# Optimization experiments

Hardware: AMD Instinct MI355X
Metric: run time of the kernel (lower is better)

## Reference

```python
import jax, jax.numpy as jnp
import numpy as np

STRIDE = 3


def _conv_block(x, W, b):
    # x: (B, L, C) -> windows (B, L-2, 3C) via fixed-stride slicing (faithful to scan_conv)
    B, L, C = x.shape
    Lw = L - STRIDE + 1
    win = jnp.concatenate([x[:, i:Lw + i, :] for i in range(STRIDE)], axis=-1)  # (B, Lw, 3C)
    y = jax.nn.leaky_relu(jnp.einsum('blk,ok->blo', win, W) + b)  # torch Linear: x @ W.T + b
    # zero_gate: zero rows of the *window* tensor zero the output
    mask = (jnp.sum(win, axis=2, keepdims=True) != 0).astype(y.dtype)
    y = y * mask
    # max_pool1d over sequence, kernel=2 stride=2 (floor)
    Lp = y.shape[1] // 2
    y = y[:, :2 * Lp, :].reshape(B, Lp, 2, -1).max(axis=2)
    return y


def setup_inputs() -> dict:
    key = jax.random.key(0)
    ks = jax.random.split(key, 16)
    B, PAD, E, IMG, V = 1024, 30, 512, 2048, 32000
    c1, c2, c3, lin2 = 200, 300, 300, 400
    lin1_in = 2 * c3 + IMG  # flattened (B,2,300) + image -> 600 + 2048
    s = 0.02
    return {
        'image_vectors': jax.random.normal(ks[0], (B, IMG), jnp.float32),
        'sentences': jax.random.randint(ks[1], (B, PAD), 0, V, jnp.int32),
        'embed_table': jax.random.normal(ks[2], (V, E), jnp.float32),
        'W1': jax.random.normal(ks[3], (c1, E * STRIDE), jnp.float32) * s,
        'b1': jnp.zeros((c1,), jnp.float32),
        'W2': jax.random.normal(ks[4], (c2, c1 * STRIDE), jnp.float32) * s,
        'b2': jnp.zeros((c2,), jnp.float32),
        'W3': jax.random.normal(ks[5], (c3, c2 * STRIDE), jnp.float32) * s,
        'b3': jnp.zeros((c3,), jnp.float32),
        'Wm': jax.random.normal(ks[6], (lin2, lin1_in), jnp.float32) * s,
        'bm': jnp.zeros((lin2,), jnp.float32),
        'Wo': jax.random.normal(ks[7], (1, lin2), jnp.float32) * s,
        'bo': jnp.zeros((1,), jnp.float32),
    }


def reference(image_vectors, sentences, embed_table, W1, b1, W2, b2, W3, b3, Wm, bm, Wo, bo):
    x = embed_table[sentences]                       # (B, 30, 512)
    x = _conv_block(x, W1, b1)                       # (B, 14, 200)
    x = _conv_block(x, W2, b2)                       # (B, 6, 300)
    x = _conv_block(x, W3, b3)                       # (B, 2, 300)
    B = x.shape[0]
    feats = jnp.concatenate([x.reshape(B, -1), image_vectors], axis=1)  # (B, 2648)
    h = jax.nn.leaky_relu(feats @ Wm.T + bm)         # (B, 400)
    out = h @ Wo.T + bo                              # (B, 1)
    return out
```

## Files before the change

### kernel.cpp

```cpp
#include <hip/hip_runtime.h>
#include <hip/hip_bf16.h>

#define LEAKY(v) ((v) > 0.0f ? (v) : 0.01f * (v))

constexpr int B_   = 1024;
constexpr int PAD  = 30;
constexpr int E    = 512;
constexpr int IMG  = 2048;
constexpr int C1   = 200;
constexpr int C2   = 300;
constexpr int C3   = 300;
constexpr int LIN2 = 400;

constexpr int NT1P = 16, KT1 = 48;
constexpr int NT2P = 20, KT2 = 21;
constexpr int NT3P = 24, KT3 = 30;
constexpr int NTMP = 28, KTM = 83;
constexpr int FK  = 2656;

constexpr int T1 = NT1P * KT1;
constexpr int T2 = NT2P * KT2;
constexpr int T3 = NT3P * KT3;
constexpr int TM = NTMP * KTM;
constexpr int TTOT = T1 + T2 + T3 + TM;

typedef __attribute__((ext_vector_type(8))) short bf16x8;
typedef __attribute__((ext_vector_type(4))) float f32x4;

__device__ inline unsigned short f2bf(float f) {
    __hip_bfloat16 h = __float2bfloat16(f);
    return *reinterpret_cast<unsigned short*>(&h);
}
__device__ inline float bf2f(unsigned short u) {
    unsigned int b = ((unsigned int)u) << 16;
    return __uint_as_float(b);
}

__global__ __launch_bounds__(256) void convert_all(
    const float* __restrict__ W1, const float* __restrict__ W2,
    const float* __restrict__ W3, const float* __restrict__ Wm,
    unsigned short* __restrict__ W1t, unsigned short* __restrict__ W2t,
    unsigned short* __restrict__ W3t, unsigned short* __restrict__ Wmt)
{
    int idx = blockIdx.x * 256 + threadIdx.x;
    if (idx >= TTOT * 64) return;
    int lane = idx & 63, t = idx >> 6;
    unsigned short v[8];

    if (t < T1) {
        int kk = t % KT1, nt = t / KT1;
        int ch = nt * 16 + (lane & 15);
        int k0 = kk * 32 + (lane >> 4) * 8;
        #pragma unroll
        for (int j = 0; j < 8; ++j)
            v[j] = (ch < C1) ? f2bf(W1[(size_t)ch * (3*E) + k0 + j]) : (unsigned short)0;
        ushort4* dst = reinterpret_cast<ushort4*>(W1t) + (size_t)t * 128 + lane * 2;
        dst[0] = ushort4{v[0],v[1],v[2],v[3]};
        dst[1] = ushort4{v[4],v[5],v[6],v[7]};
    } else if (t < T1 + T2) {
        int tt = t - T1;
        int kk = tt % KT2, nt = tt / KT2;
        int ch = nt * 16 + (lane & 15);
        int rowoff = kk / 7;
        int cbase  = (kk % 7) * 32 + (lane >> 4) * 8;
        #pragma unroll
        for (int j = 0; j < 8; ++j) {
            int c = cbase + j;
            v[j] = (ch < C2 && c < C1) ? f2bf(W2[(size_t)ch * (3*C1) + rowoff * C1 + c])
                                       : (unsigned short)0;
        }
        ushort4* dst = reinterpret_cast<ushort4*>(W2t) + (size_t)tt * 128 + lane * 2;
        dst[0] = ushort4{v[0],v[1],v[2],v[3]};
        dst[1] = ushort4{v[4],v[5],v[6],v[7]};
    } else if (t < T1 + T2 + T3) {
        int tt = t - T1 - T2;
        int kk = tt % KT3, nt = tt / KT3;
        int ch = nt * 16 + (lane & 15);
        int rowoff = kk / 10;
        int cbase  = (kk % 10) * 32 + (lane >> 4) * 8;
        #pragma unroll
        for (int j = 0; j < 8; ++j) {
            int c = cbase + j;
            v[j] = (ch < C3 && c < C2) ? f2bf(W3[(size_t)ch * (3*C2) + rowoff * C2 + c])
                                       : (unsigned short)0;
        }
        ushort4* dst = reinterpret_cast<ushort4*>(W3t) + (size_t)tt * 128 + lane * 2;
        dst[0] = ushort4{v[0],v[1],v[2],v[3]};
        dst[1] = ushort4{v[4],v[5],v[6],v[7]};
    } else {
        int tt = t - T1 - T2 - T3;
        int kk = tt % KTM, nt = tt / KTM;
        int ch = nt * 16 + (lane & 15);
        int kbase = kk * 32 + (lane >> 4) * 8;
        #pragma unroll
        for (int j = 0; j < 8; ++j) {
            int k = kbase + j;
            v[j] = (ch < LIN2 && k < 2648) ? f2bf(Wm[(size_t)ch * 2648 + k])
                                           : (unsigned short)0;
        }
        ushort4* dst = reinterpret_cast<ushort4*>(Wmt) + (size_t)tt * 128 + lane * 2;
        dst[0] = ushort4{v[0],v[1],v[2],v[3]};
        dst[1] = ushort4{v[4],v[5],v[6],v[7]};
    }
}

__global__ __launch_bounds__(512, 4) void conv1_mfma(
    const int* __restrict__ sent, const float* __restrict__ emb,
    const unsigned short* __restrict__ W1t, const float* __restrict__ bias,
    float* __restrict__ y)
{
    const int blk = blockIdx.x;
    const int tid = threadIdx.x;
    __shared__ unsigned short xs[66 * 512];
    __shared__ float rs[64];
    char* xsb = reinterpret_cast<char*>(xs);

    const int wid = tid >> 6, lane = tid & 63;

    for (int r = wid; r < 60; r += 8) {
        int bl = r / 30, rr = r % 30;
        int R = bl * 32 + rr;
        int row = sent[(2 * blk + bl) * PAD + rr];
        const float4* src = reinterpret_cast<const float4*>(emb + (size_t)row * E) + lane * 2;
        float4 e0 = src[0], e1 = src[1];
        float sum = e0.x + e0.y + e0.z + e0.w + e1.x + e1.y + e1.z + e1.w;
        union { ushort4 u4[2]; bf16x8 v; } pk;
        pk.u4[0] = ushort4{f2bf(e0.x), f2bf(e0.y), f2bf(e0.z), f2bf(e0.w)};
        pk.u4[1] = ushort4{f2bf(e1.x), f2bf(e1.y), f2bf(e1.z), f2bf(e1.w)};
        int byteoff = R * 1024 + ((lane ^ (R & 7)) << 4);
        *reinterpret_cast<bf16x8*>(xsb + byteoff) = pk.v;
        for (int off = 32; off; off >>= 1) sum += __shfl_down(sum, off);
        if (lane == 0) rs[R] = sum;
    }
    if (tid < 384) {
        int zi = tid >> 6;
        int R = (zi < 2) ? (30 + zi) : (60 + zi);
        int byteoff = R * 1024 + ((lane ^ (R & 7)) << 4);
        union { ushort4 u4[2]; bf16x8 v; } pk;
        pk.u4[0] = ushort4{0,0,0,0}; pk.u4[1] = ushort4{0,0,0,0};
        *reinterpret_cast<bf16x8*>(xsb + byteoff) = pk.v;
    }
    if (tid < 4) {
        const int pr[4] = {30, 31, 62, 63};
        rs[pr[tid]] = 0.f;
    }
    __syncthreads();

    const int kg = lane >> 4, trow = lane & 15, g = kg;

    const bf16x8* wb = reinterpret_cast<const bf16x8*>(W1t);
    const bf16x8* wp0 = wb + (size_t)((wid    ) * KT1) * 64 + lane;
    const bf16x8* wp1 = wb + (size_t)((wid + 8) * KT1) * 64 + lane;

    f32x4 c00={0,0,0,0},c01={0,0,0,0},c02={0,0,0,0},c03={0,0,0,0};
    f32x4 c10={0,0,0,0},c11={0,0,0,0},c12={0,0,0,0},c13={0,0,0,0};

    #pragma unroll
    for (int rowoff = 0; rowoff < 3; ++rowoff) {
        const int R0 = trow + rowoff;
        const int R1 = R0 + 16, R2 = R0 + 32, R3 = R0 + 48;
        const int b3_0 = R0 * 1024 + (((R0 & 7) ^ kg) << 4);
        const int b3_1 = R1 * 1024 + (((R1 & 7) ^ kg) << 4);
        const int b3_2 = R2 * 1024 + (((R2 & 7) ^ kg) << 4);
        const int b3_3 = R3 * 1024 + (((R3 & 7) ^ kg) << 4);
        #pragma unroll
        for (int cc = 0; cc < 16; ++cc) {
            const int kk = rowoff * 16 + cc;
            bf16x8 a0 = *reinterpret_cast<const bf16x8*>(xsb + (b3_0 ^ (cc << 6)));
            bf16x8 a1 = *reinterpret_cast<const bf16x8*>(xsb + (b3_1 ^ (cc << 6)));
            bf16x8 a2 = *reinterpret_cast<const bf16x8*>(xsb + (b3_2 ^ (cc << 6)));
            bf16x8 a3 = *reinterpret_cast<const bf16x8*>(xsb + (b3_3 ^ (cc << 6)));
            bf16x8 b0 = wp0[kk * 64];
            bf16x8 b1 = wp1[kk * 64];
            c00 = __builtin_amdgcn_mfma_f32_16x16x32_bf16(a0, b0, c00, 0, 0, 0);
            c01 = __builtin_amdgcn_mfma_f32_16x16x32_bf16(a1, b0, c01, 0, 0, 0);
            c02 = __builtin_amdgcn_mfma_f32_16x16x32_bf16(a2, b0, c02, 0, 0, 0);
            c03 = __builtin_amdgcn_mfma_f32_16x16x32_bf16(a3, b0, c03, 0, 0, 0);
            c10 = __builtin_amdgcn_mfma_f32_16x16x32_bf16(a0, b1, c10, 0, 0, 0);
            c11 = __builtin_amdgcn_mfma_f32_16x16x32_bf16(a1, b1, c11, 0, 0, 0);
            c12 = __builtin_amdgcn_mfma_f32_16x16x32_bf16(a2, b1, c12, 0, 0, 0);
            c13 = __builtin_amdgcn_mfma_f32_16x16x32_bf16(a3, b1, c13, 0, 0, 0);
        }
    }

#define EPIM1(MT, CM) do {                                                       \
    int bl = (MT) >> 1;                                                          \
    int mloc = ((MT) & 1) * 16;                                                  \
    int bb = 2 * blk + bl;                                                       \
    _Pragma("unroll")                                                            \
    for (int hf = 0; hf < 2; ++hf) {                                             \
        int wl = mloc + 4 * g + 2 * hf;                                          \
        int tp = wl >> 1;                                                        \
        if (tp < 14) {                                                           \
            float v0 = CM[2*hf] + bia, v1 = CM[2*hf+1] + bia;                    \
            v0 = LEAKY(v0); v1 = LEAKY(v1);                                      \
            int rb = bl * 32 + wl;                                               \
            if (rs[rb] + rs[rb+1] + rs[rb+2] == 0.f) v0 = 0.f;                   \
            if (rs[rb+1] + rs[rb+2] + rs[rb+3] == 0.f) v1 = 0.f;                 \
            y[(size_t)(bb * 14 + tp) * C1 + ch] = fmaxf(v0, v1);                 \
        }                                                                        \
    }                                                                            \
} while (0)

#define EPI1(NTI, CA, CB, CC, CD) do {                                           \
    int ch = (wid + 8 * (NTI)) * 16 + trow;                                      \
    if (ch < C1) {                                                               \
        float bia = bias[ch];                                                    \
        EPIM1(0, CA); EPIM1(1, CB); EPIM1(2, CC); EPIM1(3, CD);                  \
    }                                                                            \
} while (0)

    EPI1(0, c00, c01, c02, c03);
    EPI1(1, c10, c11, c12, c13);
#undef EPI1
#undef EPIM1
}

__global__ __launch_bounds__(256, 4) void conv2_mfma(
    const float* __restrict__ x, const unsigned short* __restrict__ Wt,
    const float* __restrict__ bias, float* __restrict__ y)
{
    const int b   = blockIdx.x;
    const int tid = threadIdx.x;
    __shared__ unsigned short xs[18 * 256];
    __shared__ float rs[18];
    char* xsb = reinterpret_cast<char*>(xs);

    for (int idx = tid; idx < 18 * 32; idx += 256) {
        int r = idx >> 5, ck = idx & 31;
        ushort4 lo = {0,0,0,0}, hi = {0,0,0,0};
        if (r < 14 && ck < 25) {
            const float4* src = reinterpret_cast<const float4*>(
                x + ((size_t)b * 14 + r) * C1 + ck * 8);
            float4 a = src[0], c = src[1];
            lo = ushort4{f2bf(a.x),f2bf(a.y),f2bf(a.z),f2bf(a.w)};
            hi = ushort4{f2bf(c.x),f2bf(c.y),f2bf(c.z),f2bf(c.w)};
        }
        int bo_ = r * 512 + ((ck ^ (r & 7)) << 4);
        *reinterpret_cast<ushort4*>(xsb + bo_)     = lo;
        *reinterpret_cast<ushort4*>(xsb + bo_ + 8) = hi;
    }
    __syncthreads();

    const int wid = tid >> 6, lane = tid & 63;
    const int kg = lane >> 4, trow = lane & 15, g = kg;

    for (int r = wid; r < 18; r += 4) {
        float s = 0.f;
        #pragma unroll
        for (int j = 0; j < 4; ++j) {
            int e = lane + 64 * j;
            int chunk = e >> 3, within = e & 7;
            s += bf2f(*reinterpret_cast<unsigned short*>(
                xsb + r * 512 + ((chunk ^ (r & 7)) << 4) + within * 2));
        }
        for (int off = 32; off; off >>= 1) s += __shfl_down(s, off);
        if (lane == 0) rs[r] = s;
    }
    __syncthreads();

    const bf16x8* wb = reinterpret_cast<const bf16x8*>(Wt);
    const bf16x8* wp0 = wb + (size_t)((wid     ) * KT2) * 64 + lane;
    const bf16x8* wp1 = wb + (size_t)((wid +  4) * KT2) * 64 + lane;
    const bf16x8* wp2 = wb + (size_t)((wid +  8) * KT2) * 64 + lane;
    const bf16x8* wp3 = wb + (size_t)((wid + 12) * KT2) * 64 + lane;
    const bf16x8* wp4 = wb + (size_t)((wid + 16) * KT2) * 64 + lane;

    f32x4 d0={0,0,0,0},d1={0,0,0,0},d2={0,0,0,0},d3={0,0,0,0},d4={0,0,0,0};

    int kidx = 0;
    #pragma unroll
    for (int rowoff = 0; rowoff < 3; ++rowoff) {
        const int R0 = trow + rowoff;
        const int b3 = R0 * 512 + (((R0 & 7) ^ kg) << 4);
        #pragma unroll
        for (int cc = 0; cc < 7; ++cc, ++kidx) {
            bf16x8 a0 = *reinterpret_cast<const bf16x8*>(xsb + (b3 ^ (cc << 6)));
            bf16x8 b0 = wp0[kidx * 64];
            bf16x8 b1 = wp1[kidx * 64];
            bf16x8 b2 = wp2[kidx * 64];
            bf16x8 b3v = wp3[kidx * 64];
            bf16x8 b4 = wp4[kidx * 64];
            d0 = __builtin_amdgcn_mfma_f32_16x16x32_bf16(a0, b0,  d0, 0, 0, 0);
            d1 = __builtin_amdgcn_mfma_f32_16x16x32_bf16(a0, b1,  d1, 0, 0, 0);
            d2 = __builtin_amdgcn_mfma_f32_16x16x32_bf16(a0, b2,  d2, 0, 0, 0);
            d3 = __builtin_amdgcn_mfma_f32_16x16x32_bf16(a0, b3v, d3, 0, 0, 0);
            d4 = __builtin_amdgcn_mfma_f32_16x16x32_bf16(a0, b4,  d4, 0, 0, 0);
        }
    }

#define EPI2(NTI, DM) do {                                                       \
    int ch = (wid + 4 * (NTI)) * 16 + trow;                                      \
    if (ch < C2) {                                                               \
        float bia = bias[ch];                                                    \
        _Pragma("unroll")                                                        \
        for (int hf = 0; hf < 2; ++hf) {                                         \
            int t0 = 4 * g + 2 * hf;                                             \
            if (t0 < 12) {                                                       \
                float v0 = LEAKY(DM[2*hf]   + bia);                              \
                float v1 = LEAKY(DM[2*hf+1] + bia);                              \
                if (rs[t0] + rs[t0+1] + rs[t0+2] == 0.f) v0 = 0.f;               \
                if (rs[t0+1] + rs[t0+2] + rs[t0+3] == 0.f) v1 = 0.f;             \
                y[((size_t)b * 6 + (t0 >> 1)) * C2 + ch] = fmaxf(v0, v1);        \
            }                                                                    \
        }                                                                        \
    }                                                                            \
} while (0)

    EPI2(0, d0);
    EPI2(1, d1);
    EPI2(2, d2);
    EPI2(3, d3);
    EPI2(4, d4);
#undef EPI2
}

__global__ __launch_bounds__(512, 4) void conv3_mfma(
    const float* __restrict__ x, const unsigned short* __restrict__ Wt,
    const float* __restrict__ bias, float* __restrict__ y)
{
    const int b0  = blockIdx.x * 4;
    const int tid = threadIdx.x;
    __shared__ unsigned short xs[24 * 320];
    __shared__ float rs[24];
    char* xsb = reinterpret_cast<char*>(xs);

    for (int idx = tid; idx < 24 * 40; idx += 512) {
        int rg = idx / 40, ck = idx % 40;
        int c0 = ck * 8;
        ushort4 lo = {0,0,0,0}, hi = {0,0,0,0};
        const float* row = x + ((size_t)b0 * 6 + rg) * C2;
        if (c0 + 8 <= C2) {
            const float4* src = reinterpret_cast<const float4*>(row + c0);
            float4 a = src[0], c = src[1];
            lo = ushort4{f2bf(a.x),f2bf(a.y),f2bf(a.z),f2bf(a.w)};
            hi = ushort4{f2bf(c.x),f2bf(c.y),f2bf(c.z),f2bf(c.w)};
        } else if (c0 < C2) {
            unsigned short v[8];
            #pragma unroll
            for (int j = 0; j < 8; ++j)
                v[j] = (c0 + j < C2) ? f2bf(row[c0 + j]) : (unsigned short)0;
            lo = ushort4{v[0],v[1],v[2],v[3]};
            hi = ushort4{v[4],v[5],v[6],v[7]};
        }
        int bo_ = rg * 640 + ((ck ^ (rg & 7)) << 4);
        *reinterpret_cast<ushort4*>(xsb + bo_)     = lo;
        *reinterpret_cast<ushort4*>(xsb + bo_ + 8) = hi;
    }
    __syncthreads();

    const int wid = tid >> 6, lane = tid & 63;
    const int kg = lane >> 4, trow = lane & 15, g = kg;

    for (int r = wid; r < 24; r += 8) {
        float s = 0.f;
        #pragma unroll
        for (int j = 0; j < 5; ++j) {
            int e = lane + 64 * j;
            int chunk = e >> 3, within = e & 7;
            s += bf2f(*reinterpret_cast<unsigned short*>(
                xsb + r * 640 + ((chunk ^ (r & 7)) << 4) + within * 2));
        }
        for (int off = 32; off; off >>= 1) s += __shfl_down(s, off);
        if (lane == 0) rs[r] = s;
    }
    __syncthreads();

    const int rbase = 6 * (trow >> 2) + (trow & 3);

    const bf16x8* wb = reinterpret_cast<const bf16x8*>(Wt);
    const bf16x8* wp0 = wb + (size_t)((wid     ) * KT3) * 64 + lane;
    const bf16x8* wp1 = wb + (size_t)((wid +  8) * KT3) * 64 + lane;
    const bf16x8* wp2 = wb + (size_t)((wid + 16) * KT3) * 64 + lane;

    f32x4 e0={0,0,0,0},e1={0,0,0,0},e2={0,0,0,0};

    int kidx = 0;
    #pragma unroll
    for (int rowoff = 0; rowoff < 3; ++rowoff) {
        const int R0 = rbase + rowoff;
        #pragma unroll
        for (int cc = 0; cc < 10; ++cc, ++kidx) {
            int chunk = cc * 4 + kg;
            bf16x8 a0 = *reinterpret_cast<const bf16x8*>(
                xsb + R0 * 640 + ((chunk ^ (R0 & 7)) << 4));
            bf16x8 b0 = wp0[kidx * 64];
            bf16x8 b1 = wp1[kidx * 64];
            bf16x8 b2 = wp2[kidx * 64];
            e0 = __builtin_amdgcn_mfma_f32_16x16x32_bf16(a0, b0, e0, 0, 0, 0);
            e1 = __builtin_amdgcn_mfma_f32_16x16x32_bf16(a0, b1, e1, 0, 0, 0);
            e2 = __builtin_amdgcn_mfma_f32_16x16x32_bf16(a0, b2, e2, 0, 0, 0);
        }
    }

#define EPI3(NTI, EM) do {                                                       \
    int ch = (wid + 8 * (NTI)) * 16 + trow;                                      \
    if (ch < C3) {                                                               \
        float bia = bias[ch];                                                    \
        _Pragma("unroll")                                                        \
        for (int tp = 0; tp < 2; ++tp) {                                         \
            int rb = g * 6 + 2 * tp;                                             \
            float v0 = LEAKY(EM[2*tp]   + bia);                                  \
            float v1 = LEAKY(EM[2*tp+1] + bia);                                  \
            if (rs[rb] + rs[rb+1] + rs[rb+2] == 0.f) v0 = 0.f;                   \
            if (rs[rb+1] + rs[rb+2] + rs[rb+3] == 0.f) v1 = 0.f;                 \
            y[((size_t)(b0 + g) * 2 + tp) * C3 + ch] = fmaxf(v0, v1);            \
        }                                                                        \
    }                                                                            \
} while (0)

    EPI3(0, e0);
    EPI3(1, e1);
    EPI3(2, e2);
#undef EPI3
}

__global__ __launch_bounds__(256) void concat_feats(
    const float* __restrict__ y3, const float* __restrict__ img,
    unsigned short* __restrict__ feats)
{
    const int b = blockIdx.x;
    for (int ck = threadIdx.x; ck < FK / 8; ck += 256) {
        int c0 = ck * 8;
        ushort4 lo = {0,0,0,0}, hi = {0,0,0,0};
        const float4* src = nullptr;
        if (c0 + 8 <= 600)       src = reinterpret_cast<const float4*>(y3 + (size_t)b*600 + c0);
        else if (c0 + 8 <= 2648) src = reinterpret_cast<const float4*>(img + (size_t)b*IMG + (c0-600));
        if (src) {
            float4 a = src[0], c = src[1];
            lo = ushort4{f2bf(a.x),f2bf(a.y),f2bf(a.z),f2bf(a.w)};
            hi = ushort4{f2bf(c.x),f2bf(c.y),f2bf(c.z),f2bf(c.w)};
        }
        ushort4* dst = reinterpret_cast<ushort4*>(feats + (size_t)b * FK + c0);
        dst[0] = lo; dst[1] = hi;
    }
}

__global__ __launch_bounds__(64) void final_mfma(
    const unsigned short* __restrict__ feats, const unsigned short* __restrict__ Wmt,
    const float* __restrict__ bm, float* __restrict__ h)
{
    const int lane = threadIdx.x;
    const int bid  = blockIdx.x;
    const int mt = bid / 7, q = bid % 7;
    const int kg = lane >> 4, trow = lane & 15, g = kg;
    const int m0 = mt * 16;

    const bf16x8* ap = reinterpret_cast<const bf16x8*>(feats)
                       + (size_t)(m0 + trow) * (FK / 8) + kg;
    const bf16x8* wb = reinterpret_cast<const bf16x8*>(Wmt);
    const bf16x8* wp0 = wb + (size_t)((q     ) * KTM) * 64 + lane;
    const bf16x8* wp1 = wb + (size_t)((q +  7) * KTM) * 64 + lane;
    const bf16x8* wp2 = wb + (size_t)((q + 14) * KTM) * 64 + lane;
    const bf16x8* wp3 = wb + (size_t)((q + 21) * KTM) * 64 + lane;

    f32x4 c0 = {0,0,0,0}, c1 = {0,0,0,0}, c2 = {0,0,0,0}, c3 = {0,0,0,0};

    bf16x8 aA = ap[0],      aB = ap[4];
    bf16x8 b0A = wp0[0],  b1A = wp1[0],  b2A = wp2[0],  b3A = wp3[0];
    bf16x8 b0B = wp0[64], b1B = wp1[64], b2B = wp2[64], b3B = wp3[64];
    for (int kk = 0; kk < KTM - 2; ++kk) {
        bf16x8 a = aA, b0 = b0A, b1 = b1A, b2 = b2A, b3 = b3A;
        aA = aB;  b0A = b0B; b1A = b1B; b2A = b2B; b3A = b3B;
        aB  = ap [(kk + 2) * 4];
        b0B = wp0[(kk + 2) * 64];
        b1B = wp1[(kk + 2) * 64];
        b2B = wp2[(kk + 2) * 64];
        b3B = wp3[(kk + 2) * 64];
        c0 = __builtin_amdgcn_mfma_f32_16x16x32_bf16(a, b0, c0, 0, 0, 0);
        c1 = __builtin_amdgcn_mfma_f32_16x16x32_bf16(a, b1, c1, 0, 0, 0);
        c2 = __builtin_amdgcn_mfma_f32_16x16x32_bf16(a, b2, c2, 0, 0, 0);
        c3 = __builtin_amdgcn_mfma_f32_16x16x32_bf16(a, b3, c3, 0, 0, 0);
    }
    c0 = __builtin_amdgcn_mfma_f32_16x16x32_bf16(aA, b0A, c0, 0, 0, 0);
    c1 = __builtin_amdgcn_mfma_f32_16x16x32_bf16(aA, b1A, c1, 0, 0, 0);
    c2 = __builtin_amdgcn_mfma_f32_16x16x32_bf16(aA, b2A, c2, 0, 0, 0);
    c3 = __builtin_amdgcn_mfma_f32_16x16x32_bf16(aA, b3A, c3, 0, 0, 0);
    c0 = __builtin_amdgcn_mfma_f32_16x16x32_bf16(aB, b0B, c0, 0, 0, 0);
    c1 = __builtin_amdgcn_mfma_f32_16x16x32_bf16(aB, b1B, c1, 0, 0, 0);
    c2 = __builtin_amdgcn_mfma_f32_16x16x32_bf16(aB, b2B, c2, 0, 0, 0);
    c3 = __builtin_amdgcn_mfma_f32_16x16x32_bf16(aB, b3B, c3, 0, 0, 0);

#define EPIM(NT, CM) do {                                                        \
    int ch = (NT) * 16 + trow;                                                   \
    if (ch < LIN2) {                                                             \
        float bia = bm[ch];                                                      \
        _Pragma("unroll")                                                        \
        for (int reg = 0; reg < 4; ++reg) {                                      \
            float v = LEAKY(CM[reg] + bia);                                      \
            h[(size_t)(m0 + 4 * g + reg) * LIN2 + ch] = v;                       \
        }                                                                        \
    }                                                                            \
} while (0)

    EPIM(q,      c0);
    EPIM(q + 7,  c1);
    EPIM(q + 14, c2);
    EPIM(q + 21, c3);
#undef EPIM
}

__global__ __launch_bounds__(256) void final_reduce(
    const float* __restrict__ h, const float* __restrict__ Wo,
    const float* __restrict__ bo, float* __restrict__ out)
{
    const int tid = threadIdx.x;
    const int wid = tid >> 6, lane = tid & 63;
    const int b = blockIdx.x * 4 + wid;
    float s = 0.f;
    #pragma unroll
    for (int j = 0; j < 7; ++j) {
        int o = lane + 64 * j;
        if (o < LIN2) s += h[(size_t)b * LIN2 + o] * Wo[o];
    }
    for (int off = 32; off; off >>= 1) s += __shfl_down(s, off);
    if (lane == 0) out[b] = s + bo[0];
}

extern "C" void kernel_launch(void* const* d_in, const int* in_sizes, int n_in,
                              void* d_out, int out_size, void* d_ws, size_t ws_size,
                              hipStream_t stream) {
    const float* image = (const float*)d_in[0];
    const int*   sent  = (const int*)  d_in[1];
    const float* emb   = (const float*)d_in[2];
    const float* W1    = (const float*)d_in[3];
    const float* b1    = (const float*)d_in[4];
    const float* W2    = (const float*)d_in[5];
    const float* b2    = (const float*)d_in[6];
    const float* W3    = (const float*)d_in[7];
    const float* b3    = (const float*)d_in[8];
    const float* Wm    = (const float*)d_in[9];
    const float* bm    = (const float*)d_in[10];
    const float* Wo    = (const float*)d_in[11];
    const float* bo    = (const float*)d_in[12];
    float* out = (float*)d_out;

    float* y1 = (float*)d_ws;
    float* y2 = y1 + 2867200;
    float* y3 = y2 + 1843200;
    unsigned short* W1t = (unsigned short*)(y3 + 614400);
    unsigned short* W2t = W1t + (size_t)T1 * 512;
    unsigned short* W3t = W2t + (size_t)T2 * 512;
    unsigned short* Wmt = W3t + (size_t)T3 * 512;
    unsigned short* feats = (unsigned short*)y1;
    float* h = y2;

    convert_all<<<(TTOT * 64 + 255) / 256, 256, 0, stream>>>(
        W1, W2, W3, Wm, W1t, W2t, W3t, Wmt);

    conv1_mfma<<<B_ / 2, 512, 0, stream>>>(sent, emb, W1t, b1, y1);
    conv2_mfma<<<B_, 256, 0, stream>>>(y1, W2t, b2, y2);
    conv3_mfma<<<B_ / 4, 512, 0, stream>>>(y2, W3t, b3, y3);
    concat_feats<<<B_, 256, 0, stream>>>(y3, image, feats);
    final_mfma<<<64 * 7, 64, 0, stream>>>(feats, Wmt, bm, h);
    final_reduce<<<B_ / 4, 256, 0, stream>>>(h, Wo, bo, out);
}
```

Baseline: 99.04 us.

## Retile conv1, conv2 and final GEMM to cut wasted tiles and raise parallelism

conv1 now has warps 5-7 skip their second N-tile, which lay entirely past the 200 output channels and only did padding work. conv2 handles two batch rows per block, so each loaded weight fragment feeds two MFMAs and weight traffic per sample halves. The final GEMM gives each wave two N-tiles instead of four and packs four waves per block, doubling the number of waves to improve latency hiding. In exchange, each final-GEMM wave reloads its A fragments across more waves, and conv2 uses more LDS per block with half as many blocks.

```diff
diff --git a/kernel.cpp b/kernel.cpp
--- a/kernel.cpp
+++ b/kernel.cpp
@@ -155,31 +155,56 @@
     f32x4 c00={0,0,0,0},c01={0,0,0,0},c02={0,0,0,0},c03={0,0,0,0};
     f32x4 c10={0,0,0,0},c11={0,0,0,0},c12={0,0,0,0},c13={0,0,0,0};
 
-    #pragma unroll
-    for (int rowoff = 0; rowoff < 3; ++rowoff) {
-        const int R0 = trow + rowoff;
-        const int R1 = R0 + 16, R2 = R0 + 32, R3 = R0 + 48;
-        const int b3_0 = R0 * 1024 + (((R0 & 7) ^ kg) << 4);
-        const int b3_1 = R1 * 1024 + (((R1 & 7) ^ kg) << 4);
-        const int b3_2 = R2 * 1024 + (((R2 & 7) ^ kg) << 4);
-        const int b3_3 = R3 * 1024 + (((R3 & 7) ^ kg) << 4);
-        #pragma unroll
-        for (int cc = 0; cc < 16; ++cc) {
-            const int kk = rowoff * 16 + cc;
-            bf16x8 a0 = *reinterpret_cast<const bf16x8*>(xsb + (b3_0 ^ (cc << 6)));
-            bf16x8 a1 = *reinterpret_cast<const bf16x8*>(xsb + (b3_1 ^ (cc << 6)));
-            bf16x8 a2 = *reinterpret_cast<const bf16x8*>(xsb + (b3_2 ^ (cc << 6)));
-            bf16x8 a3 = *reinterpret_cast<const bf16x8*>(xsb + (b3_3 ^ (cc << 6)));
-            bf16x8 b0 = wp0[kk * 64];
-            bf16x8 b1 = wp1[kk * 64];
-            c00 = __builtin_amdgcn_mfma_f32_16x16x32_bf16(a0, b0, c00, 0, 0, 0);
-            c01 = __builtin_amdgcn_mfma_f32_16x16x32_bf16(a1, b0, c01, 0, 0, 0);
-            c02 = __builtin_amdgcn_mfma_f32_16x16x32_bf16(a2, b0, c02, 0, 0, 0);
-            c03 = __builtin_amdgcn_mfma_f32_16x16x32_bf16(a3, b0, c03, 0, 0, 0);
-            c10 = __builtin_amdgcn_mfma_f32_16x16x32_bf16(a0, b1, c10, 0, 0, 0);
-            c11 = __builtin_amdgcn_mfma_f32_16x16x32_bf16(a1, b1, c11, 0, 0, 0);
-            c12 = __builtin_amdgcn_mfma_f32_16x16x32_bf16(a2, b1, c12, 0, 0, 0);
-            c13 = __builtin_amdgcn_mfma_f32_16x16x32_bf16(a3, b1, c13, 0, 0, 0);
+    if (wid < 5) {
+        #pragma unroll
+        for (int rowoff = 0; rowoff < 3; ++rowoff) {
+            const int R0 = trow + rowoff;
+            const int R1 = R0 + 16, R2 = R0 + 32, R3 = R0 + 48;
+            const int b3_0 = R0 * 1024 + (((R0 & 7) ^ kg) << 4);
+            const int b3_1 = R1 * 1024 + (((R1 & 7) ^ kg) << 4);
+            const int b3_2 = R2 * 1024 + (((R2 & 7) ^ kg) << 4);
+            const int b3_3 = R3 * 1024 + (((R3 & 7) ^ kg) << 4);
+            #pragma unroll
+            for (int cc = 0; cc < 16; ++cc) {
+                const int kk = rowoff * 16 + cc;
+                bf16x8 a0 = *reinterpret_cast<const bf16x8*>(xsb + (b3_0 ^ (cc << 6)));
+                bf16x8 a1 = *reinterpret_cast<const bf16x8*>(xsb + (b3_1 ^ (cc << 6)));
+                bf16x8 a2 = *reinterpret_cast<const bf16x8*>(xsb + (b3_2 ^ (cc << 6)));
+                bf16x8 a3 = *reinterpret_cast<const bf16x8*>(xsb + (b3_3 ^ (cc << 6)));
+                bf16x8 b0 = wp0[kk * 64];
+                bf16x8 b1 = wp1[kk * 64];
+                c00 = __builtin_amdgcn_mfma_f32_16x16x32_bf16(a0, b0, c00, 0, 0, 0);
+                c01 = __builtin_amdgcn_mfma_f32_16x16x32_bf16(a1, b0, c01, 0, 0, 0);
+                c02 = __builtin_amdgcn_mfma_f32_16x16x32_bf16(a2, b0, c02, 0, 0, 0);
+                c03 = __builtin_amdgcn_mfma_f32_16x16x32_bf16(a3, b0, c03, 0, 0, 0);
+                c10 = __builtin_amdgcn_mfma_f32_16x16x32_bf16(a0, b1, c10, 0, 0, 0);
+                c11 = __builtin_amdgcn_mfma_f32_16x16x32_bf16(a1, b1, c11, 0, 0, 0);
+                c12 = __builtin_amdgcn_mfma_f32_16x16x32_bf16(a2, b1, c12, 0, 0, 0);
+                c13 = __builtin_amdgcn_mfma_f32_16x16x32_bf16(a3, b1, c13, 0, 0, 0);
+            }
+        }
+    } else {
+        #pragma unroll
+        for (int rowoff = 0; rowoff < 3; ++rowoff) {
+            const int R0 = trow + rowoff;
+            const int R1 = R0 + 16, R2 = R0 + 32, R3 = R0 + 48;
+            const int b3_0 = R0 * 1024 + (((R0 & 7) ^ kg) << 4);
+            const int b3_1 = R1 * 1024 + (((R1 & 7) ^ kg) << 4);
+            const int b3_2 = R2 * 1024 + (((R2 & 7) ^ kg) << 4);
+            const int b3_3 = R3 * 1024 + (((R3 & 7) ^ kg) << 4);
+            #pragma unroll
+            for (int cc = 0; cc < 16; ++cc) {
+                const int kk = rowoff * 16 + cc;
+                bf16x8 a0 = *reinterpret_cast<const bf16x8*>(xsb + (b3_0 ^ (cc << 6)));
+                bf16x8 a1 = *reinterpret_cast<const bf16x8*>(xsb + (b3_1 ^ (cc << 6)));
+                bf16x8 a2 = *reinterpret_cast<const bf16x8*>(xsb + (b3_2 ^ (cc << 6)));
+                bf16x8 a3 = *reinterpret_cast<const bf16x8*>(xsb + (b3_3 ^ (cc << 6)));
+                bf16x8 b0 = wp0[kk * 64];
+                c00 = __builtin_amdgcn_mfma_f32_16x16x32_bf16(a0, b0, c00, 0, 0, 0);
+                c01 = __builtin_amdgcn_mfma_f32_16x16x32_bf16(a1, b0, c01, 0, 0, 0);
+                c02 = __builtin_amdgcn_mfma_f32_16x16x32_bf16(a2, b0, c02, 0, 0, 0);
+                c03 = __builtin_amdgcn_mfma_f32_16x16x32_bf16(a3, b0, c03, 0, 0, 0);
+            }
         }
     }
 
@@ -211,7 +236,9 @@
 } while (0)
 
     EPI1(0, c00, c01, c02, c03);
-    EPI1(1, c10, c11, c12, c13);
+    if (wid < 5) {
+        EPI1(1, c10, c11, c12, c13);
+    }
 #undef EPI1
 #undef EPIM1
 }
@@ -220,23 +247,24 @@
     const float* __restrict__ x, const unsigned short* __restrict__ Wt,
     const float* __restrict__ bias, float* __restrict__ y)
 {
-    const int b   = blockIdx.x;
+    const int blk = blockIdx.x;
     const int tid = threadIdx.x;
-    __shared__ unsigned short xs[18 * 256];
-    __shared__ float rs[18];
+    __shared__ unsigned short xs[36 * 256];
+    __shared__ float rs[36];
     char* xsb = reinterpret_cast<char*>(xs);
 
-    for (int idx = tid; idx < 18 * 32; idx += 256) {
-        int r = idx >> 5, ck = idx & 31;
+    for (int idx = tid; idx < 36 * 32; idx += 256) {
+        int rg = idx >> 5, ck = idx & 31;
+        int bl = rg / 18, r = rg % 18;
         ushort4 lo = {0,0,0,0}, hi = {0,0,0,0};
         if (r < 14 && ck < 25) {
             const float4* src = reinterpret_cast<const float4*>(
-                x + ((size_t)b * 14 + r) * C1 + ck * 8);
+                x + ((size_t)(2 * blk + bl) * 14 + r) * C1 + ck * 8);
             float4 a = src[0], c = src[1];
             lo = ushort4{f2bf(a.x),f2bf(a.y),f2bf(a.z),f2bf(a.w)};
             hi = ushort4{f2bf(c.x),f2bf(c.y),f2bf(c.z),f2bf(c.w)};
         }
-        int bo_ = r * 512 + ((ck ^ (r & 7)) << 4);
+        int bo_ = rg * 512 + ((ck ^ (rg & 7)) << 4);
         *reinterpret_cast<ushort4*>(xsb + bo_)     = lo;
         *reinterpret_cast<ushort4*>(xsb + bo_ + 8) = hi;
     }
@@ -245,7 +273,7 @@
     const int wid = tid >> 6, lane = tid & 63;
     const int kg = lane >> 4, trow = lane & 15, g = kg;
 
-    for (int r = wid; r < 18; r += 4) {
+    for (int r = wid; r < 36; r += 4) {
         float s = 0.f;
         #pragma unroll
         for (int j = 0; j < 4; ++j) {
@@ -266,30 +294,42 @@
     const bf16x8* wp3 = wb + (size_t)((wid + 12) * KT2) * 64 + lane;
     const bf16x8* wp4 = wb + (size_t)((wid + 16) * KT2) * 64 + lane;
 
-    f32x4 d0={0,0,0,0},d1={0,0,0,0},d2={0,0,0,0},d3={0,0,0,0},d4={0,0,0,0};
+    f32x4 d00={0,0,0,0},d01={0,0,0,0};
+    f32x4 d10={0,0,0,0},d11={0,0,0,0};
+    f32x4 d20={0,0,0,0},d21={0,0,0,0};
+    f32x4 d30={0,0,0,0},d31={0,0,0,0};
+    f32x4 d40={0,0,0,0},d41={0,0,0,0};
 
     int kidx = 0;
     #pragma unroll
     for (int rowoff = 0; rowoff < 3; ++rowoff) {
         const int R0 = trow + rowoff;
-        const int b3 = R0 * 512 + (((R0 & 7) ^ kg) << 4);
+        const int R1 = R0 + 18;
+        const int b3_0 = R0 * 512 + (((R0 & 7) ^ kg) << 4);
+        const int b3_1 = R1 * 512 + (((R1 & 7) ^ kg) << 4);
         #pragma unroll
         for (int cc = 0; cc < 7; ++cc, ++kidx) {
-            bf16x8 a0 = *reinterpret_cast<const bf16x8*>(xsb + (b3 ^ (cc << 6)));
+            bf16x8 a0 = *reinterpret_cast<const bf16x8*>(xsb + (b3_0 ^ (cc << 6)));
+            bf16x8 a1 = *reinterpret_cast<const bf16x8*>(xsb + (b3_1 ^ (cc << 6)));
             bf16x8 b0 = wp0[kidx * 64];
             bf16x8 b1 = wp1[kidx * 64];
             bf16x8 b2 = wp2[kidx * 64];
-            bf16x8 b3v = wp3[kidx * 64];
+            bf16x8 b3 = wp3[kidx * 64];
             bf16x8 b4 = wp4[kidx * 64];
-            d0 = __builtin_amdgcn_mfma_f32_16x16x32_bf16(a0, b0,  d0, 0, 0, 0);
-            d1 = __builtin_amdgcn_mfma_f32_16x16x32_bf16(a0, b1,  d1, 0, 0, 0);
-            d2 = __builtin_amdgcn_mfma_f32_16x16x32_bf16(a0, b2,  d2, 0, 0, 0);
-            d3 = __builtin_amdgcn_mfma_f32_16x16x32_bf16(a0, b3v, d3, 0, 0, 0);
-            d4 = __builtin_amdgcn_mfma_f32_16x16x32_bf16(a0, b4,  d4, 0, 0, 0);
-        }
-    }
-
-#define EPI2(NTI, DM) do {                                                       \
+            d00 = __builtin_amdgcn_mfma_f32_16x16x32_bf16(a0, b0, d00, 0, 0, 0);
+            d01 = __builtin_amdgcn_mfma_f32_16x16x32_bf16(a1, b0, d01, 0, 0, 0);
+            d10 = __builtin_amdgcn_mfma_f32_16x16x32_bf16(a0, b1, d10, 0, 0, 0);
+            d11 = __builtin_amdgcn_mfma_f32_16x16x32_bf16(a1, b1, d11, 0, 0, 0);
+            d20 = __builtin_amdgcn_mfma_f32_16x16x32_bf16(a0, b2, d20, 0, 0, 0);
+            d21 = __builtin_amdgcn_mfma_f32_16x16x32_bf16(a1, b2, d21, 0, 0, 0);
+            d30 = __builtin_amdgcn_mfma_f32_16x16x32_bf16(a0, b3, d30, 0, 0, 0);
+            d31 = __builtin_amdgcn_mfma_f32_16x16x32_bf16(a1, b3, d31, 0, 0, 0);
+            d40 = __builtin_amdgcn_mfma_f32_16x16x32_bf16(a0, b4, d40, 0, 0, 0);
+            d41 = __builtin_amdgcn_mfma_f32_16x16x32_bf16(a1, b4, d41, 0, 0, 0);
+        }
+    }
+
+#define EPI2(NTI, DA, DB) do {                                                   \
     int ch = (wid + 4 * (NTI)) * 16 + trow;                                      \
     if (ch < C2) {                                                               \
         float bia = bias[ch];                                                    \
@@ -297,21 +337,27 @@
         for (int hf = 0; hf < 2; ++hf) {                                         \
             int t0 = 4 * g + 2 * hf;                                             \
             if (t0 < 12) {                                                       \
-                float v0 = LEAKY(DM[2*hf]   + bia);                              \
-                float v1 = LEAKY(DM[2*hf+1] + bia);                              \
-                if (rs[t0] + rs[t0+1] + rs[t0+2] == 0.f) v0 = 0.f;               \
-                if (rs[t0+1] + rs[t0+2] + rs[t0+3] == 0.f) v1 = 0.f;             \
-                y[((size_t)b * 6 + (t0 >> 1)) * C2 + ch] = fmaxf(v0, v1);        \
+                { float v0 = LEAKY(DA[2*hf]   + bia);                            \
+                  float v1 = LEAKY(DA[2*hf+1] + bia);                            \
+                  if (rs[t0] + rs[t0+1] + rs[t0+2] == 0.f) v0 = 0.f;             \
+                  if (rs[t0+1] + rs[t0+2] + rs[t0+3] == 0.f) v1 = 0.f;           \
+                  y[((size_t)(2 * blk) * 6 + (t0 >> 1)) * C2 + ch] = fmaxf(v0, v1); } \
+                { float v0 = LEAKY(DB[2*hf]   + bia);                            \
+                  float v1 = LEAKY(DB[2*hf+1] + bia);                            \
+                  int rb = 18 + t0;                                              \
+                  if (rs[rb] + rs[rb+1] + rs[rb+2] == 0.f) v0 = 0.f;             \
+                  if (rs[rb+1] + rs[rb+2] + rs[rb+3] == 0.f) v1 = 0.f;           \
+                  y[((size_t)(2 * blk + 1) * 6 + (t0 >> 1)) * C2 + ch] = fmaxf(v0, v1); } \
             }                                                                    \
         }                                                                        \
     }                                                                            \
 } while (0)
 
-    EPI2(0, d0);
-    EPI2(1, d1);
-    EPI2(2, d2);
-    EPI2(3, d3);
-    EPI2(4, d4);
+    EPI2(0, d00, d01);
+    EPI2(1, d10, d11);
+    EPI2(2, d20, d21);
+    EPI2(3, d30, d31);
+    EPI2(4, d40, d41);
 #undef EPI2
 }
 
@@ -436,13 +482,14 @@
     }
 }
 
-__global__ __launch_bounds__(64) void final_mfma(
+__global__ __launch_bounds__(256) void final_mfma(
     const unsigned short* __restrict__ feats, const unsigned short* __restrict__ Wmt,
     const float* __restrict__ bm, float* __restrict__ h)
 {
-    const int lane = threadIdx.x;
-    const int bid  = blockIdx.x;
-    const int mt = bid / 7, q = bid % 7;
+    const int tid = threadIdx.x;
+    const int wid = tid >> 6, lane = tid & 63;
+    const int gw = blockIdx.x * 4 + wid;
+    const int mt = gw / 14, q = gw % 14;
     const int kg = lane >> 4, trow = lane & 15, g = kg;
     const int m0 = mt * 16;
 
@@ -450,36 +497,26 @@
                        + (size_t)(m0 + trow) * (FK / 8) + kg;
     const bf16x8* wb = reinterpret_cast<const bf16x8*>(Wmt);
     const bf16x8* wp0 = wb + (size_t)((q     ) * KTM) * 64 + lane;
-    const bf16x8* wp1 = wb + (size_t)((q +  7) * KTM) * 64 + lane;
-    const bf16x8* wp2 = wb + (size_t)((q + 14) * KTM) * 64 + lane;
-    const bf16x8* wp3 = wb + (size_t)((q + 21) * KTM) * 64 + lane;
-
-    f32x4 c0 = {0,0,0,0}, c1 = {0,0,0,0}, c2 = {0,0,0,0}, c3 = {0,0,0,0};
-
-    bf16x8 aA = ap[0],      aB = ap[4];
-    bf16x8 b0A = wp0[0],  b1A = wp1[0],  b2A = wp2[0],  b3A = wp3[0];
-    bf16x8 b0B = wp0[64], b1B = wp1[64], b2B = wp2[64], b3B = wp3[64];
+    const bf16x8* wp1 = wb + (size_t)((q + 14) * KTM) * 64 + lane;
+
+    f32x4 c0 = {0,0,0,0}, c1 = {0,0,0,0};
+
+    bf16x8 aA = ap[0],     aB = ap[4];
+    bf16x8 b0A = wp0[0],   b1A = wp1[0];
+    bf16x8 b0B = wp0[64],  b1B = wp1[64];
     for (int kk = 0; kk < KTM - 2; ++kk) {
-        bf16x8 a = aA, b0 = b0A, b1 = b1A, b2 = b2A, b3 = b3A;
-        aA = aB;  b0A = b0B; b1A = b1B; b2A = b2B; b3A = b3B;
+        bf16x8 a = aA, b0 = b0A, b1 = b1A;
+        aA = aB; b0A = b0B; b1A = b1B;
         aB  = ap [(kk + 2) * 4];
         b0B = wp0[(kk + 2) * 64];
         b1B = wp1[(kk + 2) * 64];
-        b2B = wp2[(kk + 2) * 64];
-        b3B = wp3[(kk + 2) * 64];
         c0 = __builtin_amdgcn_mfma_f32_16x16x32_bf16(a, b0, c0, 0, 0, 0);
         c1 = __builtin_amdgcn_mfma_f32_16x16x32_bf16(a, b1, c1, 0, 0, 0);
-        c2 = __builtin_amdgcn_mfma_f32_16x16x32_bf16(a, b2, c2, 0, 0, 0);
-        c3 = __builtin_amdgcn_mfma_f32_16x16x32_bf16(a, b3, c3, 0, 0, 0);
     }
     c0 = __builtin_amdgcn_mfma_f32_16x16x32_bf16(aA, b0A, c0, 0, 0, 0);
     c1 = __builtin_amdgcn_mfma_f32_16x16x32_bf16(aA, b1A, c1, 0, 0, 0);
-    c2 = __builtin_amdgcn_mfma_f32_16x16x32_bf16(aA, b2A, c2, 0, 0, 0);
-    c3 = __builtin_amdgcn_mfma_f32_16x16x32_bf16(aA, b3A, c3, 0, 0, 0);
     c0 = __builtin_amdgcn_mfma_f32_16x16x32_bf16(aB, b0B, c0, 0, 0, 0);
     c1 = __builtin_amdgcn_mfma_f32_16x16x32_bf16(aB, b1B, c1, 0, 0, 0);
-    c2 = __builtin_amdgcn_mfma_f32_16x16x32_bf16(aB, b2B, c2, 0, 0, 0);
-    c3 = __builtin_amdgcn_mfma_f32_16x16x32_bf16(aB, b3B, c3, 0, 0, 0);
 
 #define EPIM(NT, CM) do {                                                        \
     int ch = (NT) * 16 + trow;                                                   \
@@ -494,9 +531,7 @@
 } while (0)
 
     EPIM(q,      c0);
-    EPIM(q + 7,  c1);
-    EPIM(q + 14, c2);
-    EPIM(q + 21, c3);
+    EPIM(q + 14, c1);
 #undef EPIM
 }
 
@@ -549,9 +584,9 @@
         W1, W2, W3, Wm, W1t, W2t, W3t, Wmt);
 
     conv1_mfma<<<B_ / 2, 512, 0, stream>>>(sent, emb, W1t, b1, y1);
-    conv2_mfma<<<B_, 256, 0, stream>>>(y1, W2t, b2, y2);
+    conv2_mfma<<<B_ / 2, 256, 0, stream>>>(y1, W2t, b2, y2);
     conv3_mfma<<<B_ / 4, 512, 0, stream>>>(y2, W3t, b3, y3);
     concat_feats<<<B_, 256, 0, stream>>>(y3, image, feats);
-    final_mfma<<<64 * 7, 64, 0, stream>>>(feats, Wmt, bm, h);
+    final_mfma<<<224, 256, 0, stream>>>(feats, Wmt, bm, h);
     final_reduce<<<B_ / 4, 256, 0, stream>>>(h, Wo, bo, out);
 }
```

Measured after the change: 121.4 us. 22.6% more time.
